# Optimization experiments

Measured on AMD Instinct MI355X. Metric: run time of the kernel, lower is better.

## Reference

```python
import math
import jax, jax.numpy as jnp
import numpy as np

HID = 2048
H = 16
HKV = 8
D = HID // H          # 128 head_dim
F = D                 # feature_dim = head_dim
SEQ = 2048
BATCH = 2
THETA = 10000.0


def setup_inputs() -> dict:
    key = jax.random.key(0)
    ks = jax.random.split(key, 10)
    s = lambda k, shape, scale=0.02: (jax.random.normal(k, shape, dtype=jnp.float32) * scale)
    return {
        "hidden_states": jax.random.normal(ks[0], (BATCH, SEQ, HID), dtype=jnp.float32),
        "Wq": s(ks[1], (HID, HID)),
        "bq": s(ks[2], (HID,)),
        "Wk": s(ks[3], (HKV * D, HID)),
        "bk": s(ks[4], (HKV * D,)),
        "Wv": s(ks[5], (HKV * D, HID)),
        "bv": s(ks[6], (HKV * D,)),
        "Wo": s(ks[7], (HID, HID)),
        "bo": s(ks[8], (HID,)),
        "rand_matrix": jax.random.normal(ks[9], (F // 2, D), dtype=jnp.float32),
    }


def _rotate_half(x):
    x1, x2 = x[..., : x.shape[-1] // 2], x[..., x.shape[-1] // 2 :]
    return jnp.concatenate((-x2, x1), axis=-1)


def _softmax_kernel(x, R):
    # L2-normalize last dim (norm clamped at 1e-6), project, [sin, cos] features
    n = jnp.sqrt(jnp.sum(x * x, axis=-1, keepdims=True))
    x = x / jnp.maximum(n, 1e-6)
    p = jnp.einsum("...d,ed->...e", x, R)          # [..., F/2]
    feats = jnp.concatenate([jnp.sin(p), jnp.cos(p)], axis=-1)
    return feats / math.sqrt(F)


def reference(hidden_states, Wq, bq, Wk, bk, Wv, bv, Wo, bo, rand_matrix):
    b, s, _ = hidden_states.shape
    q = (hidden_states @ Wq.T + bq).reshape(b, s, H, D).transpose(0, 2, 1, 3)    # bhsd
    k = (hidden_states @ Wk.T + bk).reshape(b, s, HKV, D).transpose(0, 2, 1, 3)
    v = (hidden_states @ Wv.T + bv).reshape(b, s, HKV, D).transpose(0, 2, 1, 3)

    # RoPE (default position_ids = arange)
    inv_freq = 1.0 / (THETA ** (jnp.arange(0, D, 2, dtype=jnp.float32) / D))     # [D/2]
    freqs = jnp.arange(s, dtype=jnp.float32)[:, None] * inv_freq[None, :]        # [s, D/2]
    emb = jnp.concatenate((freqs, freqs), axis=-1)                               # [s, D]
    cos = jnp.cos(emb)[None, None, :, :]
    sin = jnp.sin(emb)[None, None, :, :]
    q = q * cos + _rotate_half(q) * sin
    k = k * cos + _rotate_half(k) * sin

    # GQA repeat (repeat_interleave along head axis)
    rep = H // HKV
    k = jnp.repeat(k, rep, axis=1)
    v = jnp.repeat(v, rep, axis=1)

    qp = _softmax_kernel(q, rand_matrix)   # [b,H,s,F]
    kp = _softmax_kernel(k, rand_matrix)   # [b,H,s,F]

    # Faithful to source einsums: contraction over the HEAD axis
    # torch: 'bsnd,bsnh->bndh' with tensors laid out (b, head, seq, dim)
    kv = jnp.einsum("bhsf,bhsd->bsfd", kp, v)        # [b, s, F, D]
    out = jnp.einsum("bhsf,bsfd->bhsd", qp, kv)      # [b, H, s, D]
    out = out.reshape(b, s, HID)                      # flat reshape, as in source
    return out @ Wo.T + bo
```

## Files before the change

kernel.cpp:

```cpp
#include <hip/hip_runtime.h>
#include <stdint.h>

typedef unsigned short ushort_t;
typedef __bf16 bf16x8 __attribute__((ext_vector_type(8)));
typedef float f32x4 __attribute__((ext_vector_type(4)));
typedef unsigned int u32;

__device__ __forceinline__ float bf2f(ushort_t u) {
    union { u32 u; float f; } x; x.u = ((u32)u) << 16; return x.f;
}
__device__ __forceinline__ ushort_t f2bf(float f) {
    union { float f; u32 u; } x; x.f = f;
    u32 r = x.u + 0x7FFFu + ((x.u >> 16) & 1u);
    return (ushort_t)(r >> 16);
}

__device__ __forceinline__ void async16(const void* gp, void* lp) {
    __builtin_amdgcn_global_load_lds(
        (const __attribute__((address_space(1))) u32*)(gp),
        (__attribute__((address_space(3))) u32*)(lp),
        16, 0, 0);
}

template<int N>
__device__ __forceinline__ void wait_barrier() {
    asm volatile("s_waitcnt vmcnt(%0)\n\ts_barrier" :: "n"(N) : "memory");
}

__global__ __launch_bounds__(256) void cast_all_kernel(
    const float* __restrict__ hs, const float* __restrict__ Wq,
    const float* __restrict__ Wk, const float* __restrict__ Wv,
    const float* __restrict__ Wo, const float* __restrict__ Rm,
    ushort_t* __restrict__ Xb, ushort_t* __restrict__ Wcat,
    ushort_t* __restrict__ Wo16, ushort_t* __restrict__ Rbf)
{
    int bid = blockIdx.x;
    const float* src; ushort_t* dst; int base;
    if (bid < 8192)       { src = hs; dst = Xb;              base = bid; }
    else if (bid < 12288) { src = Wq; dst = Wcat;            base = bid - 8192; }
    else if (bid < 14336) { src = Wk; dst = Wcat + 4194304;  base = bid - 12288; }
    else if (bid < 16384) { src = Wv; dst = Wcat + 6291456;  base = bid - 14336; }
    else if (bid < 20480) { src = Wo; dst = Wo16;            base = bid - 16384; }
    else                  { src = Rm; dst = Rbf;             base = bid - 20480; }
    int i = (base * 256 + threadIdx.x) * 4;
    float4 v = *reinterpret_cast<const float4*>(src + i);
    ushort4 o;
    o.x = f2bf(v.x); o.y = f2bf(v.y); o.z = f2bf(v.z); o.w = f2bf(v.w);
    *reinterpret_cast<ushort4*>(dst + i) = o;
}

__global__ void build_bcat_kernel(const float* __restrict__ bq,
                                  const float* __restrict__ bk,
                                  const float* __restrict__ bv,
                                  float* __restrict__ bcat)
{
    int i = blockIdx.x * 256 + threadIdx.x;
    float v = (i < 2048) ? bq[i] : (i < 3072) ? bk[i - 2048] : bv[i - 3072];
    bcat[i] = v;
}

#define CLOSE_PLAIN __builtin_amdgcn_s_barrier()
#define CLOSE_VM(nn) do { asm volatile("s_waitcnt vmcnt(%0)" :: "n"(nn) : "memory"); \
                          __builtin_amdgcn_s_barrier(); } while (0)

template<int BM, int MBLK, int NBLK, int KC, bool STORE_BF16>
__global__ __launch_bounds__(512, 2) void gemm8p_kernel(
    const ushort_t* __restrict__ A, const ushort_t* __restrict__ B,
    const float* __restrict__ bias, void* __restrict__ C,
    const int M, const int N)
{
    constexpr int NT  = KC / 64;
    constexpr int NI  = NT / 2;
    constexpr int MF2 = BM / 64;
    constexpr int NFR = BM / 32;
    constexpr int AH  = BM * 64;
    constexpr int SH  = BM / 128;
    constexpr int BUF = 2 * AH + 32768;
    constexpr int TI  = 2 * SH + 4;
    static_assert(NT % 2 == 0 && NI >= 3, "need even NT >= 6");
    __shared__ alignas(16) char lds[2 * BUF];

    const int tid  = threadIdx.x;
    const int wid  = tid >> 6;
    const int lane = tid & 63;
    const int wm = wid >> 2, wn = wid & 3;

    constexpr int XN  = NBLK / 8;
    constexpr int NXR = 8 / XN;
    constexpr int RH  = MBLK / NXR;
    const int x  = blockIdx.x & 7;
    const int kb = blockIdx.x >> 3;
    const int mb = (x % NXR) * RH + (kb >> 3);
    const int nb = (x / NXR) * 8 + (kb & 7);
    const int am0 = mb * BM, bn0 = nb * 256;

    const int sr3 = tid >> 3;
    const int c8  = tid & 7;
    const int cs  = c8 ^ (sr3 & 7);
    const long K2 = (long)KC * 2;
    const char* agp = (const char*)A + (size_t)(am0 + sr3) * K2 + cs * 16;
    const char* bgp = (const char*)B + (size_t)(bn0 + sr3) * K2 + cs * 16;
    const int ldsw = wid << 10;

    const int fr = lane & 15, fc = lane >> 4;
    const int sw0 = ((fc)     ^ (fr & 7)) * 16;
    const int sw1 = ((4 + fc) ^ (fr & 7)) * 16;
    const int abase = wm * AH + fr * 128;
    const int bbase = 2 * AH + wn * 8192 + fr * 128;

    f32x4 acc[NFR][4] = {};
    bf16x8 bf[4];

    auto stage_half = [&](const char* gp, int rowoff, int bufb, int off,
                          long kof, int niss) {
        char* lp = lds + bufb + off + ldsw;
        const char* g = gp + (size_t)rowoff * K2 + kof;
#pragma unroll
        for (int i = 0; i < niss; ++i)
            async16(g + (size_t)(i * 64) * K2, lp + i * 8192);
    };
#define SA0(T) stage_half(agp, 0,      ((T) & 1) * BUF, 0,          (long)(T) * 128, SH)
#define SA1(T) stage_half(agp, BM / 2, ((T) & 1) * BUF, AH,         (long)(T) * 128, SH)
#define SB0(T) stage_half(bgp, 0,      ((T) & 1) * BUF, 2 * AH,     (long)(T) * 128, 2)
#define SB1(T) stage_half(bgp, 128,    ((T) & 1) * BUF, 2 * AH + 16384, (long)(T) * 128, 2)

#define PH(h, kc, bufb, STG, CLOSE) do {                                      \
    const char* lp_ = lds + (bufb);                                           \
    const int sw_ = (kc) ? sw1 : sw0;                                         \
    if ((h) == 0) {                                                           \
        _Pragma("unroll") for (int n = 0; n < 4; ++n)                         \
            bf[n] = *(const bf16x8*)(lp_ + bbase + n * 2048 + sw_);           \
    }                                                                         \
    bf16x8 af_[MF2];                                                          \
    _Pragma("unroll") for (int j = 0; j < MF2; ++j)                           \
        af_[j] = *(const bf16x8*)(lp_ + abase + ((h) * MF2 + j) * 2048 + sw_);\
    STG;                                                                      \
    __builtin_amdgcn_s_barrier();                                             \
    asm volatile("s_waitcnt lgkmcnt(0)" ::: "memory");                        \
    __builtin_amdgcn_s_setprio(1);                                            \
    _Pragma("unroll") for (int j = 0; j < MF2; ++j)                           \
    _Pragma("unroll") for (int n = 0; n < 4; ++n)                             \
        acc[(h) * MF2 + j][n] = __builtin_amdgcn_mfma_f32_16x16x32_bf16(      \
            af_[j], bf[n], acc[(h) * MF2 + j][n], 0, 0, 0);                   \
    __builtin_amdgcn_s_setprio(0);                                            \
    CLOSE;                                                                    \
} while (0)

    SA0(0); SA1(0); SB0(0); SB1(0);
    SA0(1); SA1(1); SB0(1); SB1(1);
    wait_barrier<TI>();

    PH(0, 0, 0,    (void)0,  CLOSE_PLAIN);
    PH(1, 0, 0,    (void)0,  CLOSE_PLAIN);
    PH(0, 1, 0,    (void)0,  CLOSE_PLAIN);
    PH(1, 1, 0,    SB0(2),   CLOSE_VM(2));
    PH(0, 0, BUF,  SB1(2),   CLOSE_PLAIN);
    PH(1, 0, BUF,  SA0(2),   CLOSE_PLAIN);
    PH(0, 1, BUF,  SA1(2),   CLOSE_PLAIN);
    PH(1, 1, BUF,  SB0(3),   CLOSE_VM(2));

    for (int i = 1; i <= NI - 2; ++i) {
        const int t = 2 * i;
        PH(0, 0, 0,    SB1(t + 1), CLOSE_PLAIN);
        PH(1, 0, 0,    SA0(t + 1), CLOSE_PLAIN);
        PH(0, 1, 0,    SA1(t + 1), CLOSE_PLAIN);
        PH(1, 1, 0,    SB0(t + 2), CLOSE_VM(2));
        PH(0, 0, BUF,  SB1(t + 2), CLOSE_PLAIN);
        PH(1, 0, BUF,  SA0(t + 2), CLOSE_PLAIN);
        PH(0, 1, BUF,  SA1(t + 2), CLOSE_PLAIN);
        PH(1, 1, BUF,  SB0(t + 3), CLOSE_VM(2));
    }

    {
        constexpr int T1 = NT - 1;
        PH(0, 0, 0,    SB1(T1),  CLOSE_PLAIN);
        PH(1, 0, 0,    SA0(T1),  CLOSE_PLAIN);
        PH(0, 1, 0,    SA1(T1),  CLOSE_PLAIN);
        PH(1, 1, 0,    (void)0,  CLOSE_VM(0));
        PH(0, 0, BUF,  (void)0,  CLOSE_PLAIN);
        PH(1, 0, BUF,  (void)0,  CLOSE_PLAIN);
        PH(0, 1, BUF,  (void)0,  CLOSE_PLAIN);
        PH(1, 1, BUF,  (void)0,  CLOSE_PLAIN);
    }

    const int crow0 = fc << 2;
#pragma unroll
    for (int m = 0; m < NFR; ++m) {
        const int row_b = am0 + wm * (BM / 2) + m * 16 + crow0;
#pragma unroll
        for (int n = 0; n < 4; ++n) {
            const int col = bn0 + wn * 64 + n * 16 + fr;
            const float bs = bias[col];
#pragma unroll
            for (int r = 0; r < 4; ++r) {
                const float v = acc[m][n][r] + bs;
                if (STORE_BF16)
                    ((ushort_t*)C)[(size_t)(row_b + r) * N + col] = f2bf(v);
                else
                    ((float*)C)[(size_t)(row_b + r) * N + col] = v;
            }
        }
    }
#undef PH
#undef SA0
#undef SA1
#undef SB0
#undef SB1
}

__global__ __launch_bounds__(256) void rope_norm_kernel(
    const ushort_t* __restrict__ qkv, ushort_t* __restrict__ xnorm)
{
    const int tok = blockIdx.x;
    const int s = tok & 2047;
    const int wid = threadIdx.x >> 6, lane = threadIdx.x & 63;

    float invf = exp2f(-(float)lane * (13.287712379549449f / 64.0f));
    float ang = (float)s * invf;
    float sn, cs;
    sincosf(ang, &sn, &cs);

    const ushort_t* row = qkv + (size_t)tok * 4096;
#pragma unroll
    for (int i = 0; i < 6; ++i) {
        int vec = wid * 6 + i;
        int base = (vec < 16) ? vec * 128 : 2048 + (vec - 16) * 128;
        float a = bf2f(row[base + lane]);
        float c = bf2f(row[base + lane + 64]);
        float ra = a * cs - c * sn;
        float rc = c * cs + a * sn;
        float ss2 = ra * ra + rc * rc;
#pragma unroll
        for (int off = 32; off; off >>= 1) ss2 += __shfl_xor(ss2, off);
        float inv = 1.0f / fmaxf(sqrtf(ss2), 1e-6f);
        ushort_t* orow = xnorm + (size_t)tok * 3072 + vec * 128;
        orow[lane]      = f2bf(ra * inv);
        orow[lane + 64] = f2bf(rc * inv);
    }
}

__global__ __launch_bounds__(256) void feats_kernel(
    ushort_t* __restrict__ xnorm, const ushort_t* __restrict__ Rbf)
{
    const int wid = threadIdx.x >> 6, lane = threadIdx.x & 63;
    const int r0 = blockIdx.x * 128 + wid * 32;
    const int fr = lane & 15, fk = (lane >> 4) << 3;

    bf16x8 bfv[4][4];
#pragma unroll
    for (int n = 0; n < 4; ++n)
#pragma unroll
        for (int kk = 0; kk < 4; ++kk)
            bfv[n][kk] = *reinterpret_cast<const bf16x8*>(
                Rbf + (n * 16 + fr) * 128 + kk * 32 + fk);

    f32x4 acc[2][4] = {};
#pragma unroll
    for (int m = 0; m < 2; ++m) {
#pragma unroll
        for (int kk = 0; kk < 4; ++kk) {
            bf16x8 af = *reinterpret_cast<const bf16x8*>(
                xnorm + (size_t)(r0 + m * 16 + fr) * 128 + kk * 32 + fk);
#pragma unroll
            for (int n = 0; n < 4; ++n)
                acc[m][n] = __builtin_amdgcn_mfma_f32_16x16x32_bf16(
                    af, bfv[n][kk], acc[m][n], 0, 0, 0);
        }
    }

    const int crow0 = (lane >> 4) << 2;
#pragma unroll
    for (int m = 0; m < 2; ++m)
#pragma unroll
        for (int n = 0; n < 4; ++n) {
            int e = n * 16 + fr;
#pragma unroll
            for (int r = 0; r < 4; ++r) {
                int row = r0 + m * 16 + crow0 + r;
                float p = acc[m][n][r];
                float sp, cp;
                sincosf(p, &sp, &cp);
                ushort_t* orow = xnorm + (size_t)row * 128;
                orow[e]      = f2bf(sp * 0.08838834764831845f);
                orow[e + 64] = f2bf(cp * 0.08838834764831845f);
            }
        }
}

__global__ __launch_bounds__(256) void ctx_kernel(
    const ushort_t* __restrict__ feats, const ushort_t* __restrict__ qkv,
    ushort_t* __restrict__ ctx)
{
    __shared__ float qp[16][132];
    __shared__ float kp[8][132];
    __shared__ float vsm[8][132];
    __shared__ float Apart[2][16][8];
    __shared__ float Am[16][8];

    const int tok = blockIdx.x;
    const int b = tok >> 11, s = tok & 2047;
    const int tid = threadIdx.x;
    const ushort_t* frow = feats + (size_t)tok * 3072;
    const ushort_t* vrow = qkv + (size_t)tok * 4096 + 3072;

    for (int idx = tid; idx < 3072; idx += 256) {
        int vec = idx >> 7, d = idx & 127;
        float f = bf2f(frow[idx]);
        if (vec < 16) qp[vec][d] = f; else kp[vec - 16][d] = f;
    }
    for (int idx = tid; idx < 1024; idx += 256)
        vsm[idx >> 7][idx & 127] = bf2f(vrow[idx]);
    __syncthreads();

    {
        int half = tid >> 7, pid = tid & 127;
        int h = pid >> 3, hk = pid & 7;
        int f0 = half * 64;
        float acc = 0.f;
#pragma unroll
        for (int f = 0; f < 64; f += 4) {
            float4 qa = *reinterpret_cast<const float4*>(&qp[h][f0 + f]);
            float4 ka = *reinterpret_cast<const float4*>(&kp[hk][f0 + f]);
            acc = fmaf(qa.x, ka.x, acc); acc = fmaf(qa.y, ka.y, acc);
            acc = fmaf(qa.z, ka.z, acc); acc = fmaf(qa.w, ka.w, acc);
        }
        Apart[half][h][hk] = acc;
    }
    __syncthreads();
    if (tid < 128) {
        int h = tid >> 3, hk = tid & 7;
        Am[h][hk] = 2.0f * (Apart[0][h][hk] + Apart[1][h][hk]);
    }
    __syncthreads();

    for (int idx = tid; idx < 2048; idx += 256) {
        int h = idx >> 7, d = idx & 127;
        float acc = 0.f;
#pragma unroll
        for (int hk = 0; hk < 8; ++hk) acc = fmaf(Am[h][hk], vsm[hk][d], acc);
        int row = (b << 11) + (h << 7) + (s >> 4);
        int col = ((s & 15) << 7) + d;
        ctx[(size_t)row * 2048 + col] = f2bf(acc);
    }
}

extern "C" void kernel_launch(void* const* d_in, const int* in_sizes, int n_in,
                              void* d_out, int out_size, void* d_ws, size_t ws_size,
                              hipStream_t stream)
{
    const float* hs = (const float*)d_in[0];
    const float* Wq = (const float*)d_in[1];
    const float* bq = (const float*)d_in[2];
    const float* Wk = (const float*)d_in[3];
    const float* bk = (const float*)d_in[4];
    const float* Wv = (const float*)d_in[5];
    const float* bv = (const float*)d_in[6];
    const float* Wo = (const float*)d_in[7];
    const float* bo = (const float*)d_in[8];
    const float* Rm = (const float*)d_in[9];
    float* out = (float*)d_out;

    char* ws = (char*)d_ws;
    ushort_t* Xb   = (ushort_t*)(ws);
    ushort_t* Wcat = (ushort_t*)(ws + 16777216);
    ushort_t* Wo16 = (ushort_t*)(ws + 33554432);
    ushort_t* qkv  = (ushort_t*)(ws + 41943040);
    ushort_t* ctx  = (ushort_t*)(ws + 75497472);
    float*    bcat = (float*)   (ws + 92274688);
    ushort_t* Rbf  = (ushort_t*)(ws + 92291072);
    ushort_t* xnorm = (ushort_t*)(ws);

    cast_all_kernel<<<20488, 256, 0, stream>>>(hs, Wq, Wk, Wv, Wo, Rm,
                                               Xb, Wcat, Wo16, Rbf);
    build_bcat_kernel<<<16, 256, 0, stream>>>(bq, bk, bv, bcat);

    gemm8p_kernel<256, 16, 16, 2048, true><<<256, 512, 0, stream>>>(
        Xb, Wcat, bcat, qkv, 4096, 4096);

    rope_norm_kernel<<<4096, 256, 0, stream>>>(qkv, xnorm);
    feats_kernel<<<768, 256, 0, stream>>>(xnorm, Rbf);
    ctx_kernel<<<4096, 256, 0, stream>>>(xnorm, qkv, ctx);

    gemm8p_kernel<128, 32, 8, 2048, false><<<256, 512, 0, stream>>>(
        ctx, Wo16, bo, out, 4096, 2048);
}
```

Measured before the change: 169.1 us.

## Fuse rope/norm, feature projection and context into one per-token kernel

Merges the rope+normalize, random-feature projection and per-token context kernels into a single kernel that keeps normalized vectors and features in shared memory. This removes the global round trips of the xnorm/feature buffers and two launches. The q·k head-affinity matrix is now computed with one MFMA (k rows zero-padded) instead of scalar FMAs. The bias concat is folded into the cast kernel, which now converts 8 elements per thread. In exchange, each block reloads the projection matrix fragments from global memory and makes more shared-memory passes.

```diff
diff --git a/kernel.cpp b/kernel.cpp
--- a/kernel.cpp
+++ b/kernel.cpp
@@ -31,32 +31,34 @@
     const float* __restrict__ hs, const float* __restrict__ Wq,
     const float* __restrict__ Wk, const float* __restrict__ Wv,
     const float* __restrict__ Wo, const float* __restrict__ Rm,
+    const float* __restrict__ bq, const float* __restrict__ bk,
+    const float* __restrict__ bv,
     ushort_t* __restrict__ Xb, ushort_t* __restrict__ Wcat,
-    ushort_t* __restrict__ Wo16, ushort_t* __restrict__ Rbf)
+    ushort_t* __restrict__ Wo16, ushort_t* __restrict__ Rbf,
+    float* __restrict__ bcat)
 {
     int bid = blockIdx.x;
+    if (bid == 10244) {
+        for (int i = threadIdx.x; i < 4096; i += 256) {
+            float v = (i < 2048) ? bq[i] : (i < 3072) ? bk[i - 2048] : bv[i - 3072];
+            bcat[i] = v;
+        }
+        return;
+    }
     const float* src; ushort_t* dst; int base;
-    if (bid < 8192)       { src = hs; dst = Xb;              base = bid; }
-    else if (bid < 12288) { src = Wq; dst = Wcat;            base = bid - 8192; }
-    else if (bid < 14336) { src = Wk; dst = Wcat + 4194304;  base = bid - 12288; }
-    else if (bid < 16384) { src = Wv; dst = Wcat + 6291456;  base = bid - 14336; }
-    else if (bid < 20480) { src = Wo; dst = Wo16;            base = bid - 16384; }
-    else                  { src = Rm; dst = Rbf;             base = bid - 20480; }
-    int i = (base * 256 + threadIdx.x) * 4;
-    float4 v = *reinterpret_cast<const float4*>(src + i);
-    ushort4 o;
-    o.x = f2bf(v.x); o.y = f2bf(v.y); o.z = f2bf(v.z); o.w = f2bf(v.w);
-    *reinterpret_cast<ushort4*>(dst + i) = o;
-}
-
-__global__ void build_bcat_kernel(const float* __restrict__ bq,
-                                  const float* __restrict__ bk,
-                                  const float* __restrict__ bv,
-                                  float* __restrict__ bcat)
-{
-    int i = blockIdx.x * 256 + threadIdx.x;
-    float v = (i < 2048) ? bq[i] : (i < 3072) ? bk[i - 2048] : bv[i - 3072];
-    bcat[i] = v;
+    if (bid < 4096)       { src = hs; dst = Xb;              base = bid; }
+    else if (bid < 6144)  { src = Wq; dst = Wcat;            base = bid - 4096; }
+    else if (bid < 7168)  { src = Wk; dst = Wcat + 4194304;  base = bid - 6144; }
+    else if (bid < 8192)  { src = Wv; dst = Wcat + 6291456;  base = bid - 7168; }
+    else if (bid < 10240) { src = Wo; dst = Wo16;            base = bid - 8192; }
+    else                  { src = Rm; dst = Rbf;             base = bid - 10240; }
+    int i = base * 2048 + threadIdx.x * 8;
+    float4 v0 = *reinterpret_cast<const float4*>(src + i);
+    float4 v1 = *reinterpret_cast<const float4*>(src + i + 4);
+    ushort_t o[8];
+    o[0] = f2bf(v0.x); o[1] = f2bf(v0.y); o[2] = f2bf(v0.z); o[3] = f2bf(v0.w);
+    o[4] = f2bf(v1.x); o[5] = f2bf(v1.y); o[6] = f2bf(v1.z); o[7] = f2bf(v1.w);
+    *reinterpret_cast<uint4*>(dst + i) = *reinterpret_cast<const uint4*>(o);
 }
 
 #define CLOSE_PLAIN __builtin_amdgcn_s_barrier()
@@ -208,19 +210,25 @@
 #undef SB1
 }
 
-__global__ __launch_bounds__(256) void rope_norm_kernel(
-    const ushort_t* __restrict__ qkv, ushort_t* __restrict__ xnorm)
+__global__ __launch_bounds__(256) void fused_attn_kernel(
+    const ushort_t* __restrict__ qkv, const ushort_t* __restrict__ Rbf,
+    ushort_t* __restrict__ ctx)
 {
+    __shared__ ushort_t xnb[32][136];
+    __shared__ ushort_t fpb[32][136];
+    __shared__ float vsm[8][132];
+    __shared__ float Am[16][20];
+
     const int tok = blockIdx.x;
-    const int s = tok & 2047;
-    const int wid = threadIdx.x >> 6, lane = threadIdx.x & 63;
+    const int b = tok >> 11, s = tok & 2047;
+    const int tid = threadIdx.x;
+    const int wid = tid >> 6, lane = tid & 63;
+    const ushort_t* row = qkv + (size_t)tok * 4096;
 
     float invf = exp2f(-(float)lane * (13.287712379549449f / 64.0f));
     float ang = (float)s * invf;
     float sn, cs;
     sincosf(ang, &sn, &cs);
-
-    const ushort_t* row = qkv + (size_t)tok * 4096;
 #pragma unroll
     for (int i = 0; i < 6; ++i) {
         int vec = wid * 6 + i;
@@ -233,103 +241,54 @@
 #pragma unroll
         for (int off = 32; off; off >>= 1) ss2 += __shfl_xor(ss2, off);
         float inv = 1.0f / fmaxf(sqrtf(ss2), 1e-6f);
-        ushort_t* orow = xnorm + (size_t)tok * 3072 + vec * 128;
-        orow[lane]      = f2bf(ra * inv);
-        orow[lane + 64] = f2bf(rc * inv);
-    }
-}
-
-__global__ __launch_bounds__(256) void feats_kernel(
-    ushort_t* __restrict__ xnorm, const ushort_t* __restrict__ Rbf)
-{
-    const int wid = threadIdx.x >> 6, lane = threadIdx.x & 63;
-    const int r0 = blockIdx.x * 128 + wid * 32;
-    const int fr = lane & 15, fk = (lane >> 4) << 3;
-
-    bf16x8 bfv[4][4];
-#pragma unroll
-    for (int n = 0; n < 4; ++n)
-#pragma unroll
-        for (int kk = 0; kk < 4; ++kk)
-            bfv[n][kk] = *reinterpret_cast<const bf16x8*>(
-                Rbf + (n * 16 + fr) * 128 + kk * 32 + fk);
-
-    f32x4 acc[2][4] = {};
-#pragma unroll
-    for (int m = 0; m < 2; ++m) {
-#pragma unroll
-        for (int kk = 0; kk < 4; ++kk) {
-            bf16x8 af = *reinterpret_cast<const bf16x8*>(
-                xnorm + (size_t)(r0 + m * 16 + fr) * 128 + kk * 32 + fk);
-#pragma unroll
-            for (int n = 0; n < 4; ++n)
-                acc[m][n] = __builtin_amdgcn_mfma_f32_16x16x32_bf16(
-                    af, bfv[n][kk], acc[m][n], 0, 0, 0);
+        xnb[vec][lane]      = f2bf(ra * inv);
+        xnb[vec][lane + 64] = f2bf(rc * inv);
+    }
+    for (int idx = tid; idx < 1024; idx += 256) {
+        xnb[24 + (idx >> 7)][idx & 127] = 0;
+        vsm[idx >> 7][idx & 127] = bf2f(row[3072 + idx]);
+    }
+    __syncthreads();
+
+    {
+        const int fr = lane & 15, fc = lane >> 4;
+        f32x4 pacc[2] = {};
+#pragma unroll
+        for (int kc = 0; kc < 4; ++kc) {
+            bf16x8 bfrag = *reinterpret_cast<const bf16x8*>(
+                Rbf + (wid * 16 + fr) * 128 + kc * 32 + fc * 8);
+            bf16x8 a0 = *reinterpret_cast<const bf16x8*>(&xnb[fr][kc * 32 + fc * 8]);
+            bf16x8 a1 = *reinterpret_cast<const bf16x8*>(&xnb[16 + fr][kc * 32 + fc * 8]);
+            pacc[0] = __builtin_amdgcn_mfma_f32_16x16x32_bf16(a0, bfrag, pacc[0], 0, 0, 0);
+            pacc[1] = __builtin_amdgcn_mfma_f32_16x16x32_bf16(a1, bfrag, pacc[1], 0, 0, 0);
         }
-    }
-
-    const int crow0 = (lane >> 4) << 2;
-#pragma unroll
-    for (int m = 0; m < 2; ++m)
-#pragma unroll
-        for (int n = 0; n < 4; ++n) {
-            int e = n * 16 + fr;
+        const int e = wid * 16 + fr;
+#pragma unroll
+        for (int m = 0; m < 2; ++m)
 #pragma unroll
             for (int r = 0; r < 4; ++r) {
-                int row = r0 + m * 16 + crow0 + r;
-                float p = acc[m][n][r];
+                int vec = m * 16 + fc * 4 + r;
                 float sp, cp;
-                sincosf(p, &sp, &cp);
-                ushort_t* orow = xnorm + (size_t)row * 128;
-                orow[e]      = f2bf(sp * 0.08838834764831845f);
-                orow[e + 64] = f2bf(cp * 0.08838834764831845f);
+                sincosf(pacc[m][r], &sp, &cp);
+                fpb[vec][e]      = f2bf(sp * 0.08838834764831845f);
+                fpb[vec][e + 64] = f2bf(cp * 0.08838834764831845f);
             }
+    }
+    __syncthreads();
+
+    if (wid == 0) {
+        const int fr = lane & 15, fc = lane >> 4;
+        f32x4 aacc = {};
+#pragma unroll
+        for (int kc = 0; kc < 4; ++kc) {
+            bf16x8 qa = *reinterpret_cast<const bf16x8*>(&fpb[fr][kc * 32 + fc * 8]);
+            bf16x8 ka = *reinterpret_cast<const bf16x8*>(&fpb[16 + fr][kc * 32 + fc * 8]);
+            aacc = __builtin_amdgcn_mfma_f32_16x16x32_bf16(qa, ka, aacc, 0, 0, 0);
         }
-}
-
-__global__ __launch_bounds__(256) void ctx_kernel(
-    const ushort_t* __restrict__ feats, const ushort_t* __restrict__ qkv,
-    ushort_t* __restrict__ ctx)
-{
-    __shared__ float qp[16][132];
-    __shared__ float kp[8][132];
-    __shared__ float vsm[8][132];
-    __shared__ float Apart[2][16][8];
-    __shared__ float Am[16][8];
-
-    const int tok = blockIdx.x;
-    const int b = tok >> 11, s = tok & 2047;
-    const int tid = threadIdx.x;
-    const ushort_t* frow = feats + (size_t)tok * 3072;
-    const ushort_t* vrow = qkv + (size_t)tok * 4096 + 3072;
-
-    for (int idx = tid; idx < 3072; idx += 256) {
-        int vec = idx >> 7, d = idx & 127;
-        float f = bf2f(frow[idx]);
-        if (vec < 16) qp[vec][d] = f; else kp[vec - 16][d] = f;
-    }
-    for (int idx = tid; idx < 1024; idx += 256)
-        vsm[idx >> 7][idx & 127] = bf2f(vrow[idx]);
-    __syncthreads();
-
-    {
-        int half = tid >> 7, pid = tid & 127;
-        int h = pid >> 3, hk = pid & 7;
-        int f0 = half * 64;
-        float acc = 0.f;
-#pragma unroll
-        for (int f = 0; f < 64; f += 4) {
-            float4 qa = *reinterpret_cast<const float4*>(&qp[h][f0 + f]);
-            float4 ka = *reinterpret_cast<const float4*>(&kp[hk][f0 + f]);
-            acc = fmaf(qa.x, ka.x, acc); acc = fmaf(qa.y, ka.y, acc);
-            acc = fmaf(qa.z, ka.z, acc); acc = fmaf(qa.w, ka.w, acc);
-        }
-        Apart[half][h][hk] = acc;
-    }
-    __syncthreads();
-    if (tid < 128) {
-        int h = tid >> 3, hk = tid & 7;
-        Am[h][hk] = 2.0f * (Apart[0][h][hk] + Apart[1][h][hk]);
+        if (fr < 8)
+#pragma unroll
+            for (int r = 0; r < 4; ++r)
+                Am[fc * 4 + r][fr] = 2.0f * aacc[r];
     }
     __syncthreads();
 
@@ -338,9 +297,9 @@
         float acc = 0.f;
 #pragma unroll
         for (int hk = 0; hk < 8; ++hk) acc = fmaf(Am[h][hk], vsm[hk][d], acc);
-        int row = (b << 11) + (h << 7) + (s >> 4);
-        int col = ((s & 15) << 7) + d;
-        ctx[(size_t)row * 2048 + col] = f2bf(acc);
+        int orow = (b << 11) + (h << 7) + (s >> 4);
+        int ocol = ((s & 15) << 7) + d;
+        ctx[(size_t)orow * 2048 + ocol] = f2bf(acc);
     }
 }
 
@@ -368,18 +327,15 @@
     ushort_t* ctx  = (ushort_t*)(ws + 75497472);
     float*    bcat = (float*)   (ws + 92274688);
     ushort_t* Rbf  = (ushort_t*)(ws + 92291072);
-    ushort_t* xnorm = (ushort_t*)(ws);
-
-    cast_all_kernel<<<20488, 256, 0, stream>>>(hs, Wq, Wk, Wv, Wo, Rm,
-                                               Xb, Wcat, Wo16, Rbf);
-    build_bcat_kernel<<<16, 256, 0, stream>>>(bq, bk, bv, bcat);
+
+    cast_all_kernel<<<10245, 256, 0, stream>>>(hs, Wq, Wk, Wv, Wo, Rm,
+                                               bq, bk, bv,
+                                               Xb, Wcat, Wo16, Rbf, bcat);
 
     gemm8p_kernel<256, 16, 16, 2048, true><<<256, 512, 0, stream>>>(
         Xb, Wcat, bcat, qkv, 4096, 4096);
 
-    rope_norm_kernel<<<4096, 256, 0, stream>>>(qkv, xnorm);
-    feats_kernel<<<768, 256, 0, stream>>>(xnorm, Rbf);
-    ctx_kernel<<<4096, 256, 0, stream>>>(xnorm, qkv, ctx);
+    fused_attn_kernel<<<4096, 256, 0, stream>>>(qkv, Rbf, ctx);
 
     gemm8p_kernel<128, 32, 8, 2048, false><<<256, 512, 0, stream>>>(
         ctx, Wo16, bo, out, 4096, 2048);
```

After: 144.8 us. 14.4% less time.
